# Optimization experiments

Hardware: AMD Instinct MI355X
Metric: run time of the kernel (lower is better)

The kernel has to match this reference:

```python
import jax, jax.numpy as jnp
import numpy as np
import math

B, H, HK, Q, K, D = 2, 64, 8, 1024, 1024, 128
HIDDEN = H * D

def setup_inputs() -> dict:
    key = jax.random.key(0)
    k1, k2, k3, k4, k5 = jax.random.split(key, 5)
    xq = jax.random.normal(k1, (B, H, Q, D), dtype=jnp.float32)
    keys = jax.random.normal(k2, (B, HK, K, D), dtype=jnp.float32)
    values = jax.random.normal(k3, (B, HK, K, D), dtype=jnp.float32)
    attn_mask = jax.random.normal(k4, (B, 1, Q, K), dtype=jnp.float32)
    wo = jax.random.normal(k5, (HIDDEN, HIDDEN), dtype=jnp.float32) * 0.02
    return {"xq": xq, "keys": keys, "values": values, "attn_mask": attn_mask, "wo": wo}

def reference(xq, keys, values, attn_mask, wo):
    b, h, q, d = xq.shape
    hk = keys.shape[1]
    g = h // hk  # GQA group size
    scale = 1.0 / math.sqrt(d)
    # expand kv heads to match query heads (group_attn_matmul semantics)
    k = jnp.repeat(keys, g, axis=1)    # [b, h, K, d]
    v = jnp.repeat(values, g, axis=1)  # [b, h, K, d]
    attn = jnp.einsum('bhqd,bhkd->bhqk', xq, k) * scale + attn_mask
    attn = jax.nn.softmax(attn, axis=-1)
    out = jnp.einsum('bhqk,bhkd->bhqd', attn, v)
    # nlp_concat_heads: [b, h, q, d] -> [b, q, h*d]
    out = out.transpose(0, 2, 1, 3).reshape(b, q, h * d)
    return out @ wo
```

## Files before the change

### kernel.cpp

```cpp
#include <hip/hip_runtime.h>
#include <hip/hip_bf16.h>
#include <stdint.h>

#define NB   2
#define NH   64
#define NHK  8
#define SQ   1024
#define SK   1024
#define DH   128
#define HID  8192
#define MROWS 2048
#define NT   128

typedef unsigned short u16;
typedef __bf16 bf16_t;
typedef bf16_t bf16x8 __attribute__((ext_vector_type(8)));
typedef float  f32x4  __attribute__((ext_vector_type(4)));
typedef u16    u16x8  __attribute__((ext_vector_type(8)));
typedef u16    u16x4  __attribute__((ext_vector_type(4)));

#define DEV __device__ __forceinline__

DEV u16 f2bf(float f) {
  uint32_t u = __builtin_bit_cast(uint32_t, f);
  u += 0x7fffu + ((u >> 16) & 1u);
  return (u16)(u >> 16);
}

DEV float bf2f(u16 u) {
  return __builtin_bit_cast(float, (uint32_t)u << 16);
}

DEV bf16x8 pack8(const float* v) {
  u16x8 r;
#pragma unroll
  for (int i = 0; i < 8; ++i) r[i] = f2bf(v[i]);
  return __builtin_bit_cast(bf16x8, r);
}

DEV f32x4 mfma16(bf16x8 a, bf16x8 b, f32x4 c) {
  return __builtin_amdgcn_mfma_f32_16x16x32_bf16(a, b, c, 0, 0, 0);
}

DEV void gload_lds16(const void* g, void* l) {
  __builtin_amdgcn_global_load_lds(
      (const __attribute__((address_space(1))) void*)g,
      (__attribute__((address_space(3))) void*)l, 16, 0, 0);
}

#define BAR()  asm volatile("s_barrier" ::: "memory")
#define VMC(n) asm volatile("s_waitcnt vmcnt(" #n ")" ::: "memory")

__global__ __launch_bounds__(256) void k_prep(
    const float* __restrict__ wo, u16* __restrict__ wt,
    const float* __restrict__ keys, char* __restrict__ kf,
    const float* __restrict__ values, char* __restrict__ vf,
    const float* __restrict__ mask, char* __restrict__ mf) {
  __shared__ float tile[64][65];
  const int bid = blockIdx.x;
  const int tid = threadIdx.x;

  if (bid < 16384) {
    const int k0 = (bid & 127) * 64;
    const int n0 = (bid >> 7) * 64;
    const int r  = tid >> 4, cg = tid & 15;
#pragma unroll
    for (int p = 0; p < 4; ++p) {
      int row = r + p * 16;
      float4 v = *(const float4*)(wo + (size_t)(k0 + row) * 8192 + n0 + cg * 4);
      *(float4*)&tile[row][cg * 4] = v;
    }
    __syncthreads();
#pragma unroll
    for (int p = 0; p < 4; ++p) {
      int row = r + p * 16;
      u16x4 ov;
      ov[0] = f2bf(tile[cg * 4 + 0][row]);
      ov[1] = f2bf(tile[cg * 4 + 1][row]);
      ov[2] = f2bf(tile[cg * 4 + 2][row]);
      ov[3] = f2bf(tile[cg * 4 + 3][row]);
      *(u16x4*)(wt + (size_t)(n0 + row) * 8192 + k0 + cg * 4) = ov;
    }
  } else if (bid < 17408) {
    int g = (bid - 16384) * 256 + tid;
    int l    = g & 63;
    int blk  = (g >> 6) & 15;
    int t    = (g >> 10) & 15;
    int head = g >> 14;
    int ni = blk >> 2, c = blk & 3;
    int row = t * 64 + ni * 16 + (l & 15);
    int col = c * 32 + (l >> 4) * 8;
    const float* src = keys + ((size_t)head * 1024 + row) * 128 + col;
    float tb[8];
    *(float4*)tb       = *(const float4*)src;
    *(float4*)(tb + 4) = *(const float4*)(src + 4);
    u16x8 r;
#pragma unroll
    for (int i = 0; i < 8; ++i) r[i] = f2bf(tb[i]);
    *(u16x8*)(kf + (size_t)g * 16) = r;
  } else if (bid < 18432) {
    int g = (bid - 17408) * 256 + tid;
    int l    = g & 63;
    int blk  = (g >> 6) & 15;
    int t    = (g >> 10) & 15;
    int head = g >> 14;
    int ks = blk >> 3, nd = blk & 7;
    int k0 = t * 64 + ks * 32 + (l >> 4) * 8;
    int d  = nd * 16 + (l & 15);
    const float* src = values + (size_t)head * 131072 + (size_t)k0 * 128 + d;
    u16x8 r;
#pragma unroll
    for (int j = 0; j < 8; ++j) r[j] = f2bf(src[j * 128]);
    *(u16x8*)(vf + (size_t)g * 16) = r;
  } else {
    const float L2E = 1.4426950408889634f;
    int bid2 = bid - 18432;
    int bq = bid2 >> 9;
    int qc = (bid2 >> 4) & 31;
    int tt = bid2 & 15;
    int ni = tid >> 6, l = tid & 63;
#pragma unroll
    for (int mi = 0; mi < 2; ++mi) {
      int row = qc * 32 + mi * 16 + (l & 15);
      int col = tt * 64 + ni * 16 + (l >> 4) * 4;
      float4 v = *(const float4*)(mask + ((size_t)bq * 1024 + row) * 1024 + col);
      u16x4 r;
      r[0] = f2bf(v.x * L2E);
      r[1] = f2bf(v.y * L2E);
      r[2] = f2bf(v.z * L2E);
      r[3] = f2bf(v.w * L2E);
      *(u16x4*)(mf + ((((size_t)bq * 32 + qc) * 16 + tt) * 8 + mi * 4 + ni) * 512
                + (size_t)l * 8) = r;
    }
  }
}

__global__ __launch_bounds__(512) void k_attn(
    const float* __restrict__ xq, const char* __restrict__ kf_g,
    const char* __restrict__ vf_g, const char* __restrict__ maskf,
    u16* __restrict__ abf) {
  __shared__ char kbuf[3][16384];
  __shared__ char vbuf[3][16384];
  __shared__ char pls[32768];
  const int bid = (blockIdx.x & 7) * 64 + (blockIdx.x >> 3);
  const int tid = threadIdx.x;

  const int b = bid >> 8;
  const int h = (bid >> 2) & 63;
  const int q0 = (bid & 3) * 256;
  const int hk = h >> 3;
  const int w = tid >> 6, l = tid & 63;
  const int lr = l & 15, lg = l >> 4;
  char* pbyte = pls + w * 4096;

  bf16x8 qf[2][4];
  {
    const float* qb = xq + (((size_t)(b * NH + h) * SQ) + q0 + w * 32) * DH;
#pragma unroll
    for (int mi = 0; mi < 2; ++mi)
#pragma unroll
      for (int c = 0; c < 4; ++c) {
        const float* qp = qb + (size_t)(mi * 16 + lr) * DH + c * 32 + lg * 8;
        float t[8];
        *(float4*)t       = *(const float4*)qp;
        *(float4*)(t + 4) = *(const float4*)(qp + 4);
        qf[mi][c] = pack8(t);
      }
  }

  f32x4 o[2][8];
#pragma unroll
  for (int mi = 0; mi < 2; ++mi)
#pragma unroll
    for (int nd = 0; nd < 8; ++nd) o[mi][nd] = (f32x4){0.f, 0.f, 0.f, 0.f};
  float mrun[2] = {-1e30f, -1e30f}, lrun[2] = {0.f, 0.f};

  const char* kf_h = kf_g + (size_t)(b * NHK + hk) * 262144;
  const char* vf_h = vf_g + (size_t)(b * NHK + hk) * 262144;
  const char* mk0 = maskf +
      ((size_t)(b * 32 + (bid & 3) * 8 + w) * 16) * 4096 + (size_t)l * 8;
  const float SCALE2 = 0.08838834764831845f * 1.4426950408889634f;
  const int rswz = (lr & 7) << 4;

#define STG(src, tt, dst) do {                                                 \
    const char* s_ = (src) + (((tt) & 15) * 16384);                            \
    _Pragma("unroll")                                                          \
    for (int j_ = 0; j_ < 2; ++j_)                                             \
      gload_lds16(s_ + (w * 2 + j_) * 1024 + l * 16,                           \
                  (dst) + (w * 2 + j_) * 1024);                                \
  } while (0)

  STG(kf_h, 0, kbuf[0]);
  STG(vf_h, 0, vbuf[0]);
  STG(kf_h, 1, kbuf[1]);
  STG(vf_h, 1, vbuf[1]);
  VMC(4);
  BAR();

  int cur = 0;
  for (int t = 0; t < 16; ++t) {
    const int nx2 = (cur + 2 == 3) ? 0 : ((cur + 2 == 4) ? 1 : cur + 2);
    u16x4 mpre[2][4];
#pragma unroll
    for (int mi = 0; mi < 2; ++mi)
#pragma unroll
      for (int ni = 0; ni < 4; ++ni)
        mpre[mi][ni] =
            *(const u16x4*)(mk0 + (size_t)(t * 8 + mi * 4 + ni) * 512);

    STG(kf_h, t + 2, kbuf[nx2]);
    STG(vf_h, t + 2, vbuf[nx2]);

    f32x4 st[2][4];
#pragma unroll
    for (int mi = 0; mi < 2; ++mi)
#pragma unroll
      for (int ni = 0; ni < 4; ++ni) st[mi][ni] = (f32x4){0.f, 0.f, 0.f, 0.f};
#pragma unroll
    for (int ni = 0; ni < 4; ++ni)
#pragma unroll
      for (int c = 0; c < 4; ++c) {
        bf16x8 kfr = *(const bf16x8*)(kbuf[cur] + (ni * 4 + c) * 1024 + l * 16);
        st[0][ni] = mfma16(kfr, qf[0][c], st[0][ni]);
        st[1][ni] = mfma16(kfr, qf[1][c], st[1][ni]);
      }

#pragma unroll
    for (int mi = 0; mi < 2; ++mi) {
      float x[4][4];
#pragma unroll
      for (int ni = 0; ni < 4; ++ni)
#pragma unroll
        for (int r = 0; r < 4; ++r)
          x[ni][r] = st[mi][ni][r] * SCALE2 + bf2f(mpre[mi][ni][r]);
      float v = fmaxf(fmaxf(x[0][0], x[0][1]), fmaxf(x[0][2], x[0][3]));
#pragma unroll
      for (int ni = 1; ni < 4; ++ni)
        v = fmaxf(v, fmaxf(fmaxf(x[ni][0], x[ni][1]),
                           fmaxf(x[ni][2], x[ni][3])));
      v = fmaxf(v, __shfl_xor(v, 16));
      v = fmaxf(v, __shfl_xor(v, 32));
      if (__any(v > mrun[mi] + 11.5f)) {
        float mnew = fmaxf(mrun[mi], v);
        float fac = exp2f(mrun[mi] - mnew);
        lrun[mi] *= fac;
        mrun[mi] = mnew;
#pragma unroll
        for (int r = 0; r < 4; ++r) {
          float fr = __shfl(fac, lg * 4 + r);
#pragma unroll
          for (int nd = 0; nd < 8; ++nd) o[mi][nd][r] *= fr;
        }
      }
      float rs = 0.f;
      char* prow = pbyte + (mi * 16 + lr) * 128;
#pragma unroll
      for (int ni = 0; ni < 4; ++ni) {
        float p0 = exp2f(x[ni][0] - mrun[mi]);
        float p1 = exp2f(x[ni][1] - mrun[mi]);
        float p2 = exp2f(x[ni][2] - mrun[mi]);
        float p3 = exp2f(x[ni][3] - mrun[mi]);
        rs += (p0 + p1) + (p2 + p3);
        uint2 pk;
        pk.x = f2bf(p0) | ((uint32_t)f2bf(p1) << 16);
        pk.y = f2bf(p2) | ((uint32_t)f2bf(p3) << 16);
        *(uint2*)(prow + ((ni * 32 + lg * 8) ^ rswz)) = pk;
      }
      rs += __shfl_xor(rs, 16);
      rs += __shfl_xor(rs, 32);
      lrun[mi] += rs;
    }

#pragma unroll
    for (int ks = 0; ks < 2; ++ks) {
      bf16x8 pf0 = *(const bf16x8*)(pbyte + lr * 128 +
                                    ((ks * 64 + lg * 16) ^ rswz));
      bf16x8 pf1 = *(const bf16x8*)(pbyte + (16 + lr) * 128 +
                                    ((ks * 64 + lg * 16) ^ rswz));
#pragma unroll
      for (int nd = 0; nd < 8; ++nd) {
        bf16x8 vfr = *(const bf16x8*)(vbuf[cur] + (ks * 8 + nd) * 1024 + l * 16);
        o[0][nd] = mfma16(pf0, vfr, o[0][nd]);
        o[1][nd] = mfma16(pf1, vfr, o[1][nd]);
      }
    }

    VMC(4);
    BAR();
    cur = (cur == 2) ? 0 : cur + 1;
  }
#undef STG

#pragma unroll
  for (int mi = 0; mi < 2; ++mi) {
    float inv[4];
#pragma unroll
    for (int r = 0; r < 4; ++r) inv[r] = 1.0f / __shfl(lrun[mi], lg * 4 + r);
#pragma unroll
    for (int nd = 0; nd < 8; ++nd)
#pragma unroll
      for (int r = 0; r < 4; ++r) {
        int grow = q0 + w * 32 + mi * 16 + lg * 4 + r;
        size_t m = (size_t)b * SQ + grow;
        int col = h * DH + nd * 16 + lr;
        abf[m * HID + col] = f2bf(o[mi][nd][r] * inv[r]);
      }
  }
}

__global__ __launch_bounds__(512, 2) void k_gemm(const u16* __restrict__ A,
                                                 const u16* __restrict__ Bt,
                                                 float* __restrict__ C) {
  __shared__ char L[131072];
  const int bid = blockIdx.x;
  const int logical = (bid & 7) * 32 + (bid >> 3);
  const int m0 = (logical & 7) * 256;
  const int n0 = (logical >> 3) * 256;
  const int tid = threadIdx.x;
  const int w = tid >> 6, l = tid & 63;
  const int lr = l & 15, lg = l >> 4;
  const int wm = w >> 2, wn = w & 3;

  int srow[2], scol[2];
#pragma unroll
  for (int j = 0; j < 2; ++j) {
    int ch = j * 512 + tid;
    srow[j] = ch >> 3;
    scol[j] = (ch & 7) ^ (srow[j] & 7);
  }

  const char* Ab = (const char*)A;
  const char* Bb = (const char*)Bt;

#define STAGE(gb, row0, tt, dst) do {                                          \
    int kt_ = ((tt) < NT ? (tt) : 0) * 64;                                     \
    _Pragma("unroll")                                                          \
    for (int j_ = 0; j_ < 2; ++j_)                                             \
      gload_lds16((gb) + ((size_t)((row0) + srow[j_]) * 8192 + kt_ +           \
                          scol[j_] * 8) * 2,                                   \
                  (dst) + j_ * 8192 + (w << 10));                              \
  } while (0)

#define LDA(base, hs) do {                                                     \
    _Pragma("unroll")                                                          \
    for (int mi_ = 0; mi_ < 4; ++mi_) {                                        \
      int r_ = wm * 64 + mi_ * 16 + lr;                                        \
      _Pragma("unroll")                                                        \
      for (int ks_ = 0; ks_ < 2; ++ks_)                                        \
        bA[mi_][ks_] = *(const bf16x8*)(L + (base) + (hs) * 16384 + r_ * 128 + \
                        ((ks_ * 64 + lg * 16) ^ ((r_ & 7) << 4)));             \
    }                                                                          \
  } while (0)

#define LDB(dst, base, hs) do {                                                \
    _Pragma("unroll")                                                          \
    for (int ni_ = 0; ni_ < 2; ++ni_) {                                        \
      int r_ = wn * 32 + ni_ * 16 + lr;                                        \
      _Pragma("unroll")                                                        \
      for (int ks_ = 0; ks_ < 2; ++ks_)                                        \
        dst[ni_][ks_] = *(const bf16x8*)(L + (base) + 32768 + (hs) * 16384 +   \
                        r_ * 128 + ((ks_ * 64 + lg * 16) ^ ((r_ & 7) << 4)));  \
    }                                                                          \
  } while (0)

#define MM(mh, nh, BB) do {                                                    \
    __builtin_amdgcn_s_setprio(1);                                             \
    _Pragma("unroll")                                                          \
    for (int mi_ = 0; mi_ < 4; ++mi_)                                          \
      _Pragma("unroll")                                                        \
      for (int ni_ = 0; ni_ < 2; ++ni_)                                        \
        _Pragma("unroll")                                                      \
        for (int ks_ = 0; ks_ < 2; ++ks_)                                      \
          acc[mh][nh][mi_][ni_] =                                              \
              mfma16(bA[mi_][ks_], BB[ni_][ks_], acc[mh][nh][mi_][ni_]);       \
    __builtin_amdgcn_s_setprio(0);                                             \
  } while (0)

  f32x4 acc[2][2][4][2];
#pragma unroll
  for (int a1 = 0; a1 < 2; ++a1)
#pragma unroll
    for (int a2 = 0; a2 < 2; ++a2)
#pragma unroll
      for (int a3 = 0; a3 < 4; ++a3)
#pragma unroll
        for (int a4 = 0; a4 < 2; ++a4)
          acc[a1][a2][a3][a4] = (f32x4){0.f, 0.f, 0.f, 0.f};

  bf16x8 bA[4][2], bB0[2][2], bB1[2][2];

  STAGE(Ab, m0,       0, L + 0);
  STAGE(Bb, n0,       0, L + 32768);
  STAGE(Bb, n0 + 128, 0, L + 49152);
  STAGE(Ab, m0 + 128, 0, L + 16384);
  STAGE(Ab, m0,       1, L + 65536);
  STAGE(Bb, n0,       1, L + 65536 + 32768);
  STAGE(Bb, n0 + 128, 1, L + 65536 + 49152);
  VMC(6);
  BAR();

  for (int t = 0; t < NT; ++t) {
    const int c  = (t & 1) << 16;
    const int cn = c ^ 65536;
    STAGE(Ab, m0 + 128, t + 1, L + cn + 16384);
    LDA(c, 0);
    LDB(bB0, c, 0);
    BAR();
    MM(0, 0, bB0);
    BAR();
    STAGE(Ab, m0, t + 2, L + c + 0);
    LDB(bB1, c, 1);
    BAR();
    MM(0, 1, bB1);
    BAR();
    STAGE(Bb, n0, t + 2, L + c + 32768);
    LDA(c, 1);
    BAR();
    MM(1, 1, bB1);
    BAR();
    STAGE(Bb, n0 + 128, t + 2, L + c + 49152);
    BAR();
    MM(1, 0, bB0);
    VMC(6);
    BAR();
  }
  VMC(0);

#pragma unroll
  for (int mh = 0; mh < 2; ++mh)
#pragma unroll
    for (int nh = 0; nh < 2; ++nh)
#pragma unroll
      for (int mi = 0; mi < 4; ++mi)
#pragma unroll
        for (int ni = 0; ni < 2; ++ni)
#pragma unroll
          for (int rr = 0; rr < 4; ++rr)
            C[(size_t)(m0 + mh * 128 + wm * 64 + mi * 16 + lg * 4 + rr) * 8192 +
              n0 + nh * 128 + wn * 32 + ni * 16 + lr] = acc[mh][nh][mi][ni][rr];
#undef STAGE
#undef LDA
#undef LDB
#undef MM
}

extern "C" void kernel_launch(void* const* d_in, const int* in_sizes, int n_in,
                              void* d_out, int out_size, void* d_ws, size_t ws_size,
                              hipStream_t stream) {
  const float* xq     = (const float*)d_in[0];
  const float* keys   = (const float*)d_in[1];
  const float* values = (const float*)d_in[2];
  const float* mask   = (const float*)d_in[3];
  const float* wo     = (const float*)d_in[4];
  float* out = (float*)d_out;

  char* ws = (char*)d_ws;
  u16*  Abf = (u16*)ws;
  u16*  Wt  = (u16*)(ws + 33554432ull);
  char* Kf  = ws + 33554432ull + 134217728ull;
  char* Vf  = Kf + 4194304ull;
  char* Mf  = (char*)d_out + 62914560ull;

  hipLaunchKernelGGL(k_prep, dim3(19456), dim3(256), 0, stream,
                     wo, Wt, keys, Kf, values, Vf, mask, Mf);
  hipLaunchKernelGGL(k_attn, dim3(512), dim3(512), 0, stream,
                     xq, Kf, Vf, Mf, Abf);
  hipLaunchKernelGGL(k_gemm, dim3(256), dim3(512), 0, stream, Abf, Wt, out);
}
```

Before: 460.9 us.

## Pass softmax probabilities via lane shuffles instead of LDS and double-buffer K/V

The attention kernel stops staging the bf16 probability tile through shared memory and instead rebuilds the MFMA A-operand fragments with cross-lane shuffles. It also cuts the K/V ring from triple to double buffering and adds a launch-bounds occupancy hint. Together these reduce LDS use from 128KB to 64KB per block so more blocks can be resident. The costs are extra shuffle instructions and shorter prefetch distance, since each step now waits for all outstanding loads before the barrier.

```diff
diff --git a/kernel.cpp b/kernel.cpp
--- a/kernel.cpp
+++ b/kernel.cpp
@@ -18,6 +18,7 @@
 typedef float  f32x4  __attribute__((ext_vector_type(4)));
 typedef u16    u16x8  __attribute__((ext_vector_type(8)));
 typedef u16    u16x4  __attribute__((ext_vector_type(4)));
+typedef uint32_t u32x4 __attribute__((ext_vector_type(4)));
 
 #define DEV __device__ __forceinline__
 
@@ -135,13 +136,12 @@
   }
 }
 
-__global__ __launch_bounds__(512) void k_attn(
+__global__ __launch_bounds__(512, 4) void k_attn(
     const float* __restrict__ xq, const char* __restrict__ kf_g,
     const char* __restrict__ vf_g, const char* __restrict__ maskf,
     u16* __restrict__ abf) {
-  __shared__ char kbuf[3][16384];
-  __shared__ char vbuf[3][16384];
-  __shared__ char pls[32768];
+  __shared__ char kbuf[2][16384];
+  __shared__ char vbuf[2][16384];
   const int bid = (blockIdx.x & 7) * 64 + (blockIdx.x >> 3);
   const int tid = threadIdx.x;
 
@@ -151,7 +151,6 @@
   const int hk = h >> 3;
   const int w = tid >> 6, l = tid & 63;
   const int lr = l & 15, lg = l >> 4;
-  char* pbyte = pls + w * 4096;
 
   bf16x8 qf[2][4];
   {
@@ -180,7 +179,6 @@
   const char* mk0 = maskf +
       ((size_t)(b * 32 + (bid & 3) * 8 + w) * 16) * 4096 + (size_t)l * 8;
   const float SCALE2 = 0.08838834764831845f * 1.4426950408889634f;
-  const int rswz = (lr & 7) << 4;
 
 #define STG(src, tt, dst) do {                                                 \
     const char* s_ = (src) + (((tt) & 15) * 16384);                            \
@@ -192,14 +190,15 @@
 
   STG(kf_h, 0, kbuf[0]);
   STG(vf_h, 0, vbuf[0]);
-  STG(kf_h, 1, kbuf[1]);
-  STG(vf_h, 1, vbuf[1]);
-  VMC(4);
+  VMC(0);
   BAR();
 
-  int cur = 0;
+  const int s0 = lr + ((lg & 1) << 5);
+  const int s1 = s0 + 16;
+  const bool hi_ni = ((lg >> 1) & 1) != 0;
+
   for (int t = 0; t < 16; ++t) {
-    const int nx2 = (cur + 2 == 3) ? 0 : ((cur + 2 == 4) ? 1 : cur + 2);
+    const int cur = t & 1;
     u16x4 mpre[2][4];
 #pragma unroll
     for (int mi = 0; mi < 2; ++mi)
@@ -208,8 +207,8 @@
         mpre[mi][ni] =
             *(const u16x4*)(mk0 + (size_t)(t * 8 + mi * 4 + ni) * 512);
 
-    STG(kf_h, t + 2, kbuf[nx2]);
-    STG(vf_h, t + 2, vbuf[nx2]);
+    STG(kf_h, t + 1, kbuf[cur ^ 1]);
+    STG(vf_h, t + 1, vbuf[cur ^ 1]);
 
     f32x4 st[2][4];
 #pragma unroll
@@ -225,6 +224,7 @@
         st[1][ni] = mfma16(kfr, qf[1][c], st[1][ni]);
       }
 
+    uint32_t pkx[2][4], pky[2][4];
 #pragma unroll
     for (int mi = 0; mi < 2; ++mi) {
       float x[4][4];
@@ -253,7 +253,6 @@
         }
       }
       float rs = 0.f;
-      char* prow = pbyte + (mi * 16 + lr) * 128;
 #pragma unroll
       for (int ni = 0; ni < 4; ++ni) {
         float p0 = exp2f(x[ni][0] - mrun[mi]);
@@ -261,10 +260,8 @@
         float p2 = exp2f(x[ni][2] - mrun[mi]);
         float p3 = exp2f(x[ni][3] - mrun[mi]);
         rs += (p0 + p1) + (p2 + p3);
-        uint2 pk;
-        pk.x = f2bf(p0) | ((uint32_t)f2bf(p1) << 16);
-        pk.y = f2bf(p2) | ((uint32_t)f2bf(p3) << 16);
-        *(uint2*)(prow + ((ni * 32 + lg * 8) ^ rswz)) = pk;
+        pkx[mi][ni] = (uint32_t)f2bf(p0) | ((uint32_t)f2bf(p1) << 16);
+        pky[mi][ni] = (uint32_t)f2bf(p2) | ((uint32_t)f2bf(p3) << 16);
       }
       rs += __shfl_xor(rs, 16);
       rs += __shfl_xor(rs, 32);
@@ -273,21 +270,34 @@
 
 #pragma unroll
     for (int ks = 0; ks < 2; ++ks) {
-      bf16x8 pf0 = *(const bf16x8*)(pbyte + lr * 128 +
-                                    ((ks * 64 + lg * 16) ^ rswz));
-      bf16x8 pf1 = *(const bf16x8*)(pbyte + (16 + lr) * 128 +
-                                    ((ks * 64 + lg * 16) ^ rswz));
+      bf16x8 pf[2];
+#pragma unroll
+      for (int mi = 0; mi < 2; ++mi) {
+        uint32_t a0 = __shfl(pkx[mi][ks * 2 + 0], s0);
+        uint32_t b0 = __shfl(pkx[mi][ks * 2 + 1], s0);
+        uint32_t a1 = __shfl(pky[mi][ks * 2 + 0], s0);
+        uint32_t b1 = __shfl(pky[mi][ks * 2 + 1], s0);
+        uint32_t a2 = __shfl(pkx[mi][ks * 2 + 0], s1);
+        uint32_t b2 = __shfl(pkx[mi][ks * 2 + 1], s1);
+        uint32_t a3 = __shfl(pky[mi][ks * 2 + 0], s1);
+        uint32_t b3 = __shfl(pky[mi][ks * 2 + 1], s1);
+        u32x4 fw;
+        fw[0] = hi_ni ? b0 : a0;
+        fw[1] = hi_ni ? b1 : a1;
+        fw[2] = hi_ni ? b2 : a2;
+        fw[3] = hi_ni ? b3 : a3;
+        pf[mi] = __builtin_bit_cast(bf16x8, fw);
+      }
 #pragma unroll
       for (int nd = 0; nd < 8; ++nd) {
         bf16x8 vfr = *(const bf16x8*)(vbuf[cur] + (ks * 8 + nd) * 1024 + l * 16);
-        o[0][nd] = mfma16(pf0, vfr, o[0][nd]);
-        o[1][nd] = mfma16(pf1, vfr, o[1][nd]);
+        o[0][nd] = mfma16(pf[0], vfr, o[0][nd]);
+        o[1][nd] = mfma16(pf[1], vfr, o[1][nd]);
       }
     }
 
-    VMC(4);
-    BAR();
-    cur = (cur == 2) ? 0 : cur + 1;
+    VMC(0);
+    BAR();
   }
 #undef STG
 
```

Measured after the change: 660.0 us. +43.2%, slower.
